# Kernel optimization log

Measured on AMD Instinct MI355X. Metric: run time of the kernel, lower is better.

The kernel has to match this reference:

```python
import jax, jax.numpy as jnp
import numpy as np

VOCAB, EMBED, PROJ = 200000, 300, 128
B, S = 16, 2048


def setup_inputs() -> dict:
    key = jax.random.key(0)
    k1, k2, k3, k4, k5 = jax.random.split(key, 5)
    ext_word_ids = jax.random.randint(k1, (B, S), 0, VOCAB)
    seq_lengths = jax.random.randint(k2, (B,), 1, S + 1)  # at least 1 token per sentence
    embed = jax.random.normal(k3, (VOCAB, EMBED), dtype=jnp.float32)
    embed = embed.at[0].set(0.0)  # padding_idx = 0 row is zero
    W = jax.random.normal(k4, (PROJ, EMBED), dtype=jnp.float32) * 0.05
    b = jax.random.normal(k5, (PROJ,), dtype=jnp.float32) * 0.05
    return {"ext_word_ids": ext_word_ids, "seq_lengths": seq_lengths,
            "embed": embed, "W": W, "b": b}


def reference(ext_word_ids, seq_lengths, embed, W, b):
    # Dedup in the original is purely an optimization; math is:
    # out[b, t] = W @ embed[ids[b, t]] + b  for t < seq_lengths[b], else 0.
    x = embed[ext_word_ids]                       # [B, S, E] gather
    y = jnp.einsum('bse,pe->bsp', x, W) + b       # [B, S, P] projection
    mask = jnp.arange(y.shape[1])[None, :] < seq_lengths[:, None]  # [B, S]
    return jnp.where(mask[:, :, None], y, jnp.zeros((), y.dtype))
```

## Files before the change

### kernel.cpp

```cpp
#include <hip/hip_runtime.h>


#define E 300
#define P 128
#define S 2048
#define BS 32768
#define TM 64

typedef short bf16x8 __attribute__((ext_vector_type(8)));
typedef short bf16x4 __attribute__((ext_vector_type(4)));
typedef float f32x4 __attribute__((ext_vector_type(4)));

__device__ inline unsigned short f32_bf16_fast(float f) {
    unsigned int u = __builtin_bit_cast(unsigned int, f);
    return (unsigned short)((u + 0x8000u) >> 16);
}
__device__ inline bf16x8 cvt8(f32x4 a, f32x4 b) {
    bf16x8 r;
    r[0] = (short)f32_bf16_fast(a[0]); r[1] = (short)f32_bf16_fast(a[1]);
    r[2] = (short)f32_bf16_fast(a[2]); r[3] = (short)f32_bf16_fast(a[3]);
    r[4] = (short)f32_bf16_fast(b[0]); r[5] = (short)f32_bf16_fast(b[1]);
    r[6] = (short)f32_bf16_fast(b[2]); r[7] = (short)f32_bf16_fast(b[3]);
    return r;
}
__device__ inline bf16x4 cvt4(f32x4 a) {
    bf16x4 r;
    r[0] = (short)f32_bf16_fast(a[0]); r[1] = (short)f32_bf16_fast(a[1]);
    r[2] = (short)f32_bf16_fast(a[2]); r[3] = (short)f32_bf16_fast(a[3]);
    return r;
}

__global__ __launch_bounds__(256) void ft_main(
    const int* __restrict__ ids, const int* __restrict__ seqlen,
    const float* __restrict__ embed, const float* __restrict__ Wf,
    const float* __restrict__ bias, float* __restrict__ out)
{
    __shared__ unsigned char Wl[40960];

    const int tid  = threadIdx.x;
    const int wave = tid >> 6, lane = tid & 63;
    const int fr   = lane & 15, kg = lane >> 4;

    const int tile = blockIdx.x >> 1;
    const int ch   = blockIdx.x & 1;
    const int tok0 = tile * TM;
    const int bi0  = tok0 >> 11;
    const int t0   = tok0 & (S - 1);
    const int sl0  = seqlen[bi0];

    if (sl0 <= t0) {
        #pragma unroll
        for (int i = 0; i < 4; ++i) {
            int idx   = tid + i * 256;
            int token = tok0 + (idx >> 4);
            int c     = ch * 64 + (idx & 15) * 4;
            *(f32x4*)(out + (long long)token * P + c) = (f32x4){0.f, 0.f, 0.f, 0.f};
        }
        return;
    }

    const int token_a = tok0 + wave * 16 + fr;
    const long long id = ids[token_a];
    const float* __restrict__ rp = embed + id * (long long)E;

    bf16x8 av[10];
    #pragma unroll
    for (int s = 0; s < 9; ++s) {
        const int kb = s * 32 + kg * 8;
        f32x4 f0 = *(const f32x4*)(rp + kb);
        f32x4 f1 = *(const f32x4*)(rp + kb + 4);
        av[s] = cvt8(f0, f1);
    }
    {
        f32x4 z4 = {0.f, 0.f, 0.f, 0.f};
        f32x4 f0 = z4, f1 = z4;
        if (kg == 0)      { f0 = *(const f32x4*)(rp + 288); f1 = *(const f32x4*)(rp + 292); }
        else if (kg == 1) { f0 = *(const f32x4*)(rp + 296); }
        av[9] = cvt8(f0, f1);
    }

    const int R0 = ch * 64;
    #pragma unroll
    for (int i = 0; i < 20; ++i) {
        int g4 = tid + i * 256;
        int r  = g4 / 80;
        int c4 = g4 - r * 80;
        int c0 = c4 * 4;
        f32x4 v = {0.f, 0.f, 0.f, 0.f};
        if (c0 < 300)
            v = *(const f32x4*)(Wf + (long long)(R0 + r) * E + c0);
        int s   = c0 >> 5;
        int kgg = (c0 & 31) >> 3;
        int h   = (c0 >> 2) & 1;
        int ni  = r >> 4;
        int fr2 = r & 15;
        int off = (((s * 4 + ni) * 16 + fr2) << 6) + (kgg << 4) + (h << 3);
        *(bf16x4*)(Wl + off) = cvt4(v);
    }
    __syncthreads();

    f32x4 acc[4];
    #pragma unroll
    for (int ni = 0; ni < 4; ++ni) acc[ni] = (f32x4){0.f, 0.f, 0.f, 0.f};

    #pragma unroll
    for (int s = 0; s < 10; ++s) {
        #pragma unroll
        for (int ni = 0; ni < 4; ++ni) {
            bf16x8 bv = *(const bf16x8*)(Wl + ((((s * 4 + ni) * 16 + fr) << 6) + (kg << 4)));
            acc[ni] = __builtin_amdgcn_mfma_f32_16x16x32_bf16(av[s], bv, acc[ni], 0, 0, 0);
        }
    }

    float bs[4];
    #pragma unroll
    for (int ni = 0; ni < 4; ++ni) bs[ni] = bias[ch * 64 + ni * 16 + fr];

    #pragma unroll
    for (int j = 0; j < 4; ++j) {
        int orow  = wave * 16 + kg * 4 + j;
        int token = tok0 + orow;
        int t     = token & (S - 1);
        bool valid = (t < sl0);
        #pragma unroll
        for (int ni = 0; ni < 4; ++ni) {
            float v = valid ? (acc[ni][j] + bs[ni]) : 0.0f;
            out[(long long)token * P + ch * 64 + ni * 16 + fr] = v;
        }
    }
}

extern "C" void kernel_launch(void* const* d_in, const int* in_sizes, int n_in,
                              void* d_out, int out_size, void* d_ws, size_t ws_size,
                              hipStream_t stream) {
    const int*   ids    = (const int*)d_in[0];
    const int*   sl     = (const int*)d_in[1];
    const float* embed  = (const float*)d_in[2];
    const float* W      = (const float*)d_in[3];
    const float* bias   = (const float*)d_in[4];
    float*       out    = (float*)d_out;

    ft_main<<<(BS / TM) * 2, 256, 0, stream>>>(ids, sl, embed, W, bias, out);
}
```

Baseline: 22.73 us.

## Compact valid token tiles onto blocks and spread zero-fill evenly across blocks

Each block now computes its tile index from a prefix sum over per-sentence valid-tile counts, so the compute blocks map only onto tiles that contain valid tokens. The zero-fill of the padded tail is split evenly across all 1024 blocks as a flat range of float4 stores, so no block does only a small zero-store job. The embedding-row gather is moved after the W staging loop, ahead of the barrier. This is meant to balance load and avoid spreading compute tiles unevenly over blocks. The cost is that every block reads all sequence lengths and runs a chain of range compares for each zero store.

```diff
diff --git a/kernel.cpp b/kernel.cpp
--- a/kernel.cpp
+++ b/kernel.cpp
@@ -6,6 +6,7 @@
 #define S 2048
 #define BS 32768
 #define TM 64
+#define NB 16
 
 typedef short bf16x8 __attribute__((ext_vector_type(8)));
 typedef short bf16x4 __attribute__((ext_vector_type(4)));
@@ -40,93 +41,144 @@
     const int tid  = threadIdx.x;
     const int wave = tid >> 6, lane = tid & 63;
     const int fr   = lane & 15, kg = lane >> 4;
+    const int d    = blockIdx.x;
 
-    const int tile = blockIdx.x >> 1;
-    const int ch   = blockIdx.x & 1;
-    const int tok0 = tile * TM;
-    const int bi0  = tok0 >> 11;
-    const int t0   = tok0 & (S - 1);
-    const int sl0  = seqlen[bi0];
+    const int grp = d >> 4, sub = d & 15;
+    const int rt  = grp * 8 + (sub & 7);
+    const int ch  = sub >> 3;
 
-    if (sl0 <= t0) {
-        #pragma unroll
-        for (int i = 0; i < 4; ++i) {
-            int idx   = tid + i * 256;
-            int token = tok0 + (idx >> 4);
-            int c     = ch * 64 + (idx & 15) * 4;
-            *(f32x4*)(out + (long long)token * P + c) = (f32x4){0.f, 0.f, 0.f, 0.f};
-        }
-        return;
+    int b = -1, lt = 0, acc = 0;
+    #pragma unroll
+    for (int bb = 0; bb < NB; ++bb) {
+        int rb = (seqlen[bb] + 63) >> 6;
+        if (rt >= acc && rt < acc + rb) { b = bb; lt = rt - acc; }
+        acc += rb;
     }
 
-    const int token_a = tok0 + wave * 16 + fr;
-    const long long id = ids[token_a];
-    const float* __restrict__ rp = embed + id * (long long)E;
+    if (b >= 0) {
+        const int tok0 = (b << 11) + (lt << 6);
+        const int sl0  = seqlen[b];
 
-    bf16x8 av[10];
-    #pragma unroll
-    for (int s = 0; s < 9; ++s) {
-        const int kb = s * 32 + kg * 8;
-        f32x4 f0 = *(const f32x4*)(rp + kb);
-        f32x4 f1 = *(const f32x4*)(rp + kb + 4);
-        av[s] = cvt8(f0, f1);
-    }
-    {
-        f32x4 z4 = {0.f, 0.f, 0.f, 0.f};
-        f32x4 f0 = z4, f1 = z4;
-        if (kg == 0)      { f0 = *(const f32x4*)(rp + 288); f1 = *(const f32x4*)(rp + 292); }
-        else if (kg == 1) { f0 = *(const f32x4*)(rp + 296); }
-        av[9] = cvt8(f0, f1);
-    }
+        const int R0 = ch * 64;
+        #pragma unroll
+        for (int i = 0; i < 20; ++i) {
+            int g4 = tid + i * 256;
+            int r  = g4 / 80;
+            int c4 = g4 - r * 80;
+            int c0 = c4 * 4;
+            f32x4 v = {0.f, 0.f, 0.f, 0.f};
+            if (c0 < 300)
+                v = *(const f32x4*)(Wf + (long long)(R0 + r) * E + c0);
+            int s   = c0 >> 5;
+            int kgg = (c0 & 31) >> 3;
+            int h   = (c0 >> 2) & 1;
+            int ni  = r >> 4;
+            int fr2 = r & 15;
+            int off = (((s * 4 + ni) * 16 + fr2) << 6) + (kgg << 4) + (h << 3);
+            *(bf16x4*)(Wl + off) = cvt4(v);
+        }
 
-    const int R0 = ch * 64;
-    #pragma unroll
-    for (int i = 0; i < 20; ++i) {
-        int g4 = tid + i * 256;
-        int r  = g4 / 80;
-        int c4 = g4 - r * 80;
-        int c0 = c4 * 4;
-        f32x4 v = {0.f, 0.f, 0.f, 0.f};
-        if (c0 < 300)
-            v = *(const f32x4*)(Wf + (long long)(R0 + r) * E + c0);
-        int s   = c0 >> 5;
-        int kgg = (c0 & 31) >> 3;
-        int h   = (c0 >> 2) & 1;
-        int ni  = r >> 4;
-        int fr2 = r & 15;
-        int off = (((s * 4 + ni) * 16 + fr2) << 6) + (kgg << 4) + (h << 3);
-        *(bf16x4*)(Wl + off) = cvt4(v);
-    }
-    __syncthreads();
+        const int token_a = tok0 + wave * 16 + fr;
+        const int id = ids[token_a];
+        const float* __restrict__ rp = embed + (long long)id * E;
 
-    f32x4 acc[4];
-    #pragma unroll
-    for (int ni = 0; ni < 4; ++ni) acc[ni] = (f32x4){0.f, 0.f, 0.f, 0.f};
+        bf16x8 av[10];
+        #pragma unroll
+        for (int s = 0; s < 9; ++s) {
+            const int kb = s * 32 + kg * 8;
+            f32x4 f0 = *(const f32x4*)(rp + kb);
+            f32x4 f1 = *(const f32x4*)(rp + kb + 4);
+            av[s] = cvt8(f0, f1);
+        }
+        {
+            f32x4 z4 = {0.f, 0.f, 0.f, 0.f};
+            f32x4 f0 = z4, f1 = z4;
+            if (kg == 0)      { f0 = *(const f32x4*)(rp + 288); f1 = *(const f32x4*)(rp + 292); }
+            else if (kg == 1) { f0 = *(const f32x4*)(rp + 296); }
+            av[9] = cvt8(f0, f1);
+        }
+        __syncthreads();
 
-    #pragma unroll
-    for (int s = 0; s < 10; ++s) {
+        f32x4 acc4[4];
         #pragma unroll
-        for (int ni = 0; ni < 4; ++ni) {
-            bf16x8 bv = *(const bf16x8*)(Wl + ((((s * 4 + ni) * 16 + fr) << 6) + (kg << 4)));
-            acc[ni] = __builtin_amdgcn_mfma_f32_16x16x32_bf16(av[s], bv, acc[ni], 0, 0, 0);
+        for (int ni = 0; ni < 4; ++ni) acc4[ni] = (f32x4){0.f, 0.f, 0.f, 0.f};
+
+        #pragma unroll
+        for (int s = 0; s < 10; ++s) {
+            #pragma unroll
+            for (int ni = 0; ni < 4; ++ni) {
+                bf16x8 bv = *(const bf16x8*)(Wl + ((((s * 4 + ni) * 16 + fr) << 6) + (kg << 4)));
+                acc4[ni] = __builtin_amdgcn_mfma_f32_16x16x32_bf16(av[s], bv, acc4[ni], 0, 0, 0);
+            }
+        }
+
+        float bs[4];
+        #pragma unroll
+        for (int ni = 0; ni < 4; ++ni) bs[ni] = bias[ch * 64 + ni * 16 + fr];
+
+        #pragma unroll
+        for (int j = 0; j < 4; ++j) {
+            int orow  = wave * 16 + kg * 4 + j;
+            int token = tok0 + orow;
+            int t     = token & (S - 1);
+            bool valid = (t < sl0);
+            #pragma unroll
+            for (int ni = 0; ni < 4; ++ni) {
+                float v = valid ? (acc4[ni][j] + bs[ni]) : 0.0f;
+                out[(long long)token * P + ch * 64 + ni * 16 + fr] = v;
+            }
         }
     }
 
-    float bs[4];
-    #pragma unroll
-    for (int ni = 0; ni < 4; ++ni) bs[ni] = bias[ch * 64 + ni * 16 + fr];
+    int zp0 = 0, zp1, zp2, zp3, zp4, zp5, zp6, zp7, zp8,
+        zp9, zp10, zp11, zp12, zp13, zp14, zp15, zp16;
+    int rb0  = (seqlen[0]  + 63) >> 6,  rb1  = (seqlen[1]  + 63) >> 6,
+        rb2  = (seqlen[2]  + 63) >> 6,  rb3  = (seqlen[3]  + 63) >> 6,
+        rb4  = (seqlen[4]  + 63) >> 6,  rb5  = (seqlen[5]  + 63) >> 6,
+        rb6  = (seqlen[6]  + 63) >> 6,  rb7  = (seqlen[7]  + 63) >> 6,
+        rb8  = (seqlen[8]  + 63) >> 6,  rb9  = (seqlen[9]  + 63) >> 6,
+        rb10 = (seqlen[10] + 63) >> 6,  rb11 = (seqlen[11] + 63) >> 6,
+        rb12 = (seqlen[12] + 63) >> 6,  rb13 = (seqlen[13] + 63) >> 6,
+        rb14 = (seqlen[14] + 63) >> 6,  rb15 = (seqlen[15] + 63) >> 6;
+    zp1  = zp0  + ((S - (rb0  << 6)) << 5);
+    zp2  = zp1  + ((S - (rb1  << 6)) << 5);
+    zp3  = zp2  + ((S - (rb2  << 6)) << 5);
+    zp4  = zp3  + ((S - (rb3  << 6)) << 5);
+    zp5  = zp4  + ((S - (rb4  << 6)) << 5);
+    zp6  = zp5  + ((S - (rb5  << 6)) << 5);
+    zp7  = zp6  + ((S - (rb6  << 6)) << 5);
+    zp8  = zp7  + ((S - (rb7  << 6)) << 5);
+    zp9  = zp8  + ((S - (rb8  << 6)) << 5);
+    zp10 = zp9  + ((S - (rb9  << 6)) << 5);
+    zp11 = zp10 + ((S - (rb10 << 6)) << 5);
+    zp12 = zp11 + ((S - (rb11 << 6)) << 5);
+    zp13 = zp12 + ((S - (rb12 << 6)) << 5);
+    zp14 = zp13 + ((S - (rb13 << 6)) << 5);
+    zp15 = zp14 + ((S - (rb14 << 6)) << 5);
+    zp16 = zp15 + ((S - (rb15 << 6)) << 5);
 
-    #pragma unroll
-    for (int j = 0; j < 4; ++j) {
-        int orow  = wave * 16 + kg * 4 + j;
-        int token = tok0 + orow;
-        int t     = token & (S - 1);
-        bool valid = (t < sl0);
-        #pragma unroll
-        for (int ni = 0; ni < 4; ++ni) {
-            float v = valid ? (acc[ni][j] + bs[ni]) : 0.0f;
-            out[(long long)token * P + ch * 64 + ni * 16 + fr] = v;
-        }
+    const int zq  = zp16;
+    const int per = (zq + 1023) >> 10;
+    int q0 = d * per;
+    int q1 = q0 + per; if (q1 > zq) q1 = zq;
+
+    for (int q = q0 + tid; q < q1; q += 256) {
+        int base = 0, tk0 = 0;
+        #define ZSEL(BB, LO, HI, RB) \
+            if (q >= (LO) && q < (HI)) { base = (LO); tk0 = ((BB) << 11) + ((RB) << 6); }
+        ZSEL(0,  zp0,  zp1,  rb0)  ZSEL(1,  zp1,  zp2,  rb1)
+        ZSEL(2,  zp2,  zp3,  rb2)  ZSEL(3,  zp3,  zp4,  rb3)
+        ZSEL(4,  zp4,  zp5,  rb4)  ZSEL(5,  zp5,  zp6,  rb5)
+        ZSEL(6,  zp6,  zp7,  rb6)  ZSEL(7,  zp7,  zp8,  rb7)
+        ZSEL(8,  zp8,  zp9,  rb8)  ZSEL(9,  zp9,  zp10, rb9)
+        ZSEL(10, zp10, zp11, rb10) ZSEL(11, zp11, zp12, rb11)
+        ZSEL(12, zp12, zp13, rb12) ZSEL(13, zp13, zp14, rb13)
+        ZSEL(14, zp14, zp15, rb14) ZSEL(15, zp15, zp16, rb15)
+        #undef ZSEL
+        int lq    = q - base;
+        int token = tk0 + (lq >> 5);
+        int c     = (lq & 31) << 2;
+        *(f32x4*)(out + (long long)token * P + c) = (f32x4){0.f, 0.f, 0.f, 0.f};
     }
 }
 
```

New measurement: 19.96 us. 1.14x faster.

## Double token tile per block and spread padding zero-fill evenly across all blocks

Applied to the files above, without the earlier changes.

Raises the tile to 128 tokens so each wave computes two 16-row MFMA tiles that reuse the same shared W fragments, halving per-token W staging. Blocks are remapped in groups so the two column halves of a row tile are scheduled near each other. Zero-filling of padded rows is pulled out of per-tile early exits and split evenly across all 512 blocks through a prefix sum over the per-sequence padded lengths, which balances work between active and fully padded blocks. The cost is higher register pressure, from doubled A fragments and accumulators, and extra scalar work to compute the zero ranges.

```diff
diff --git a/kernel.cpp b/kernel.cpp
--- a/kernel.cpp
+++ b/kernel.cpp
@@ -5,7 +5,8 @@
 #define P 128
 #define S 2048
 #define BS 32768
-#define TM 64
+#define TM 128
+#define NB 16
 
 typedef short bf16x8 __attribute__((ext_vector_type(8)));
 typedef short bf16x4 __attribute__((ext_vector_type(4)));
@@ -41,92 +42,153 @@
     const int wave = tid >> 6, lane = tid & 63;
     const int fr   = lane & 15, kg = lane >> 4;
 
-    const int tile = blockIdx.x >> 1;
-    const int ch   = blockIdx.x & 1;
-    const int tok0 = tile * TM;
+    const int d   = blockIdx.x;
+    const int grp = d >> 4, sub = d & 15;
+    const int rt  = grp * 8 + (sub & 7);
+    const int ch  = sub >> 3;
+
+    const int tok0 = rt * TM;
     const int bi0  = tok0 >> 11;
     const int t0   = tok0 & (S - 1);
-    const int sl0  = seqlen[bi0];
-
-    if (sl0 <= t0) {
-        #pragma unroll
-        for (int i = 0; i < 4; ++i) {
-            int idx   = tid + i * 256;
-            int token = tok0 + (idx >> 4);
-            int c     = ch * 64 + (idx & 15) * 4;
-            *(f32x4*)(out + (long long)token * P + c) = (f32x4){0.f, 0.f, 0.f, 0.f};
-        }
-        return;
+
+    const int r_lo  = tok0 + wave * 32 + fr;
+    const int id_lo = ids[r_lo];
+    const int id_hi = ids[r_lo + 16];
+    const int sl0   = seqlen[bi0];
+
+    if (sl0 > t0) {
+        const int R0 = ch * 64;
+        #pragma unroll
+        for (int i = 0; i < 20; ++i) {
+            int g4 = tid + i * 256;
+            int r  = g4 / 80;
+            int c4 = g4 - r * 80;
+            int c0 = c4 * 4;
+            f32x4 v = {0.f, 0.f, 0.f, 0.f};
+            if (c0 < 300)
+                v = *(const f32x4*)(Wf + (long long)(R0 + r) * E + c0);
+            int s   = c0 >> 5;
+            int kgg = (c0 & 31) >> 3;
+            int h   = (c0 >> 2) & 1;
+            int ni  = r >> 4;
+            int fr2 = r & 15;
+            int off = (((s * 4 + ni) * 16 + fr2) << 6) + (kgg << 4) + (h << 3);
+            *(bf16x4*)(Wl + off) = cvt4(v);
+        }
+
+        const float* __restrict__ rpL = embed + (long long)id_lo * E;
+        const float* __restrict__ rpH = embed + (long long)id_hi * E;
+
+        bf16x8 avL[10], avH[10];
+        #pragma unroll
+        for (int s = 0; s < 9; ++s) {
+            const int kb = s * 32 + kg * 8;
+            f32x4 a0 = *(const f32x4*)(rpL + kb);
+            f32x4 a1 = *(const f32x4*)(rpL + kb + 4);
+            f32x4 b0 = *(const f32x4*)(rpH + kb);
+            f32x4 b1 = *(const f32x4*)(rpH + kb + 4);
+            avL[s] = cvt8(a0, a1);
+            avH[s] = cvt8(b0, b1);
+        }
+        {
+            f32x4 z4 = {0.f, 0.f, 0.f, 0.f};
+            f32x4 a0 = z4, a1 = z4, b0 = z4, b1 = z4;
+            if (kg == 0) {
+                a0 = *(const f32x4*)(rpL + 288); a1 = *(const f32x4*)(rpL + 292);
+                b0 = *(const f32x4*)(rpH + 288); b1 = *(const f32x4*)(rpH + 292);
+            } else if (kg == 1) {
+                a0 = *(const f32x4*)(rpL + 296);
+                b0 = *(const f32x4*)(rpH + 296);
+            }
+            avL[9] = cvt8(a0, a1);
+            avH[9] = cvt8(b0, b1);
+        }
+        __syncthreads();
+
+        f32x4 aL[4], aH[4];
+        #pragma unroll
+        for (int ni = 0; ni < 4; ++ni) {
+            aL[ni] = (f32x4){0.f, 0.f, 0.f, 0.f};
+            aH[ni] = (f32x4){0.f, 0.f, 0.f, 0.f};
+        }
+        #pragma unroll
+        for (int s = 0; s < 10; ++s) {
+            #pragma unroll
+            for (int ni = 0; ni < 4; ++ni) {
+                bf16x8 bv = *(const bf16x8*)(Wl + ((((s * 4 + ni) * 16 + fr) << 6) + (kg << 4)));
+                aL[ni] = __builtin_amdgcn_mfma_f32_16x16x32_bf16(avL[s], bv, aL[ni], 0, 0, 0);
+                aH[ni] = __builtin_amdgcn_mfma_f32_16x16x32_bf16(avH[s], bv, aH[ni], 0, 0, 0);
+            }
+        }
+
+        float bs[4];
+        #pragma unroll
+        for (int ni = 0; ni < 4; ++ni) bs[ni] = bias[ch * 64 + ni * 16 + fr];
+
+        #pragma unroll
+        for (int j = 0; j < 4; ++j) {
+            int tokL = tok0 + wave * 32 + kg * 4 + j;
+            int tokH = tokL + 16;
+            bool vL = ((tokL & (S - 1)) < sl0);
+            bool vH = ((tokH & (S - 1)) < sl0);
+            #pragma unroll
+            for (int ni = 0; ni < 4; ++ni) {
+                float xL = vL ? (aL[ni][j] + bs[ni]) : 0.0f;
+                float xH = vH ? (aH[ni][j] + bs[ni]) : 0.0f;
+                out[(long long)tokL * P + ch * 64 + ni * 16 + fr] = xL;
+                out[(long long)tokH * P + ch * 64 + ni * 16 + fr] = xH;
+            }
+        }
     }
 
-    const int token_a = tok0 + wave * 16 + fr;
-    const long long id = ids[token_a];
-    const float* __restrict__ rp = embed + id * (long long)E;
-
-    bf16x8 av[10];
-    #pragma unroll
-    for (int s = 0; s < 9; ++s) {
-        const int kb = s * 32 + kg * 8;
-        f32x4 f0 = *(const f32x4*)(rp + kb);
-        f32x4 f1 = *(const f32x4*)(rp + kb + 4);
-        av[s] = cvt8(f0, f1);
-    }
-    {
-        f32x4 z4 = {0.f, 0.f, 0.f, 0.f};
-        f32x4 f0 = z4, f1 = z4;
-        if (kg == 0)      { f0 = *(const f32x4*)(rp + 288); f1 = *(const f32x4*)(rp + 292); }
-        else if (kg == 1) { f0 = *(const f32x4*)(rp + 296); }
-        av[9] = cvt8(f0, f1);
-    }
-
-    const int R0 = ch * 64;
-    #pragma unroll
-    for (int i = 0; i < 20; ++i) {
-        int g4 = tid + i * 256;
-        int r  = g4 / 80;
-        int c4 = g4 - r * 80;
-        int c0 = c4 * 4;
-        f32x4 v = {0.f, 0.f, 0.f, 0.f};
-        if (c0 < 300)
-            v = *(const f32x4*)(Wf + (long long)(R0 + r) * E + c0);
-        int s   = c0 >> 5;
-        int kgg = (c0 & 31) >> 3;
-        int h   = (c0 >> 2) & 1;
-        int ni  = r >> 4;
-        int fr2 = r & 15;
-        int off = (((s * 4 + ni) * 16 + fr2) << 6) + (kgg << 4) + (h << 3);
-        *(bf16x4*)(Wl + off) = cvt4(v);
-    }
-    __syncthreads();
-
-    f32x4 acc[4];
-    #pragma unroll
-    for (int ni = 0; ni < 4; ++ni) acc[ni] = (f32x4){0.f, 0.f, 0.f, 0.f};
-
-    #pragma unroll
-    for (int s = 0; s < 10; ++s) {
-        #pragma unroll
-        for (int ni = 0; ni < 4; ++ni) {
-            bf16x8 bv = *(const bf16x8*)(Wl + ((((s * 4 + ni) * 16 + fr) << 6) + (kg << 4)));
-            acc[ni] = __builtin_amdgcn_mfma_f32_16x16x32_bf16(av[s], bv, acc[ni], 0, 0, 0);
-        }
-    }
-
-    float bs[4];
-    #pragma unroll
-    for (int ni = 0; ni < 4; ++ni) bs[ni] = bias[ch * 64 + ni * 16 + fr];
-
-    #pragma unroll
-    for (int j = 0; j < 4; ++j) {
-        int orow  = wave * 16 + kg * 4 + j;
-        int token = tok0 + orow;
-        int t     = token & (S - 1);
-        bool valid = (t < sl0);
-        #pragma unroll
-        for (int ni = 0; ni < 4; ++ni) {
-            float v = valid ? (acc[ni][j] + bs[ni]) : 0.0f;
-            out[(long long)token * P + ch * 64 + ni * 16 + fr] = v;
-        }
+    int rb0  = (seqlen[0]  + 127) >> 7,  rb1  = (seqlen[1]  + 127) >> 7,
+        rb2  = (seqlen[2]  + 127) >> 7,  rb3  = (seqlen[3]  + 127) >> 7,
+        rb4  = (seqlen[4]  + 127) >> 7,  rb5  = (seqlen[5]  + 127) >> 7,
+        rb6  = (seqlen[6]  + 127) >> 7,  rb7  = (seqlen[7]  + 127) >> 7,
+        rb8  = (seqlen[8]  + 127) >> 7,  rb9  = (seqlen[9]  + 127) >> 7,
+        rb10 = (seqlen[10] + 127) >> 7,  rb11 = (seqlen[11] + 127) >> 7,
+        rb12 = (seqlen[12] + 127) >> 7,  rb13 = (seqlen[13] + 127) >> 7,
+        rb14 = (seqlen[14] + 127) >> 7,  rb15 = (seqlen[15] + 127) >> 7;
+    int zp0 = 0;
+    int zp1  = zp0  + ((S - (rb0  << 7)) << 5);
+    int zp2  = zp1  + ((S - (rb1  << 7)) << 5);
+    int zp3  = zp2  + ((S - (rb2  << 7)) << 5);
+    int zp4  = zp3  + ((S - (rb3  << 7)) << 5);
+    int zp5  = zp4  + ((S - (rb4  << 7)) << 5);
+    int zp6  = zp5  + ((S - (rb5  << 7)) << 5);
+    int zp7  = zp6  + ((S - (rb6  << 7)) << 5);
+    int zp8  = zp7  + ((S - (rb7  << 7)) << 5);
+    int zp9  = zp8  + ((S - (rb8  << 7)) << 5);
+    int zp10 = zp9  + ((S - (rb9  << 7)) << 5);
+    int zp11 = zp10 + ((S - (rb10 << 7)) << 5);
+    int zp12 = zp11 + ((S - (rb11 << 7)) << 5);
+    int zp13 = zp12 + ((S - (rb12 << 7)) << 5);
+    int zp14 = zp13 + ((S - (rb13 << 7)) << 5);
+    int zp15 = zp14 + ((S - (rb14 << 7)) << 5);
+    int zp16 = zp15 + ((S - (rb15 << 7)) << 5);
+
+    const int zq  = zp16;
+    const int per = (zq + 511) >> 9;
+    int q0 = d * per;
+    int q1 = q0 + per; if (q1 > zq) q1 = zq;
+
+    for (int q = q0 + tid; q < q1; q += 256) {
+        int base = 0, tk0 = 0;
+        #define ZSEL(BB, LO, HI, RB) \
+            if (q >= (LO) && q < (HI)) { base = (LO); tk0 = ((BB) << 11) + ((RB) << 7); }
+        ZSEL(0,  zp0,  zp1,  rb0)  ZSEL(1,  zp1,  zp2,  rb1)
+        ZSEL(2,  zp2,  zp3,  rb2)  ZSEL(3,  zp3,  zp4,  rb3)
+        ZSEL(4,  zp4,  zp5,  rb4)  ZSEL(5,  zp5,  zp6,  rb5)
+        ZSEL(6,  zp6,  zp7,  rb6)  ZSEL(7,  zp7,  zp8,  rb7)
+        ZSEL(8,  zp8,  zp9,  rb8)  ZSEL(9,  zp9,  zp10, rb9)
+        ZSEL(10, zp10, zp11, rb10) ZSEL(11, zp11, zp12, rb11)
+        ZSEL(12, zp12, zp13, rb12) ZSEL(13, zp13, zp14, rb13)
+        ZSEL(14, zp14, zp15, rb14) ZSEL(15, zp15, zp16, rb15)
+        #undef ZSEL
+        int lq    = q - base;
+        int token = tk0 + (lq >> 5);
+        int c     = (lq & 31) << 2;
+        *(f32x4*)(out + (long long)token * P + c) = (f32x4){0.f, 0.f, 0.f, 0.f};
     }
 }
 
```

New measurement: 23.42 us. 3.0% more time.
